# Performance work log

Measured on AMD Instinct MI355X. Metric: run time of the kernel, lower is better.

Reference implementation:

```python
import jax, jax.numpy as jnp
import numpy as np

N, H, G = 8192, 256, 256


def setup_inputs() -> dict:
    key = jax.random.key(0)
    ks = jax.random.split(key, 12)
    s = 1.0 / np.sqrt(H)
    inp = {
        "x": jax.random.normal(ks[0], (N, H), dtype=jnp.float32),
        "batch": jnp.sort(jax.random.randint(ks[1], (N,), 0, G)),
        "num_graphs": G,
        "aw": jax.random.uniform(ks[2], (H, H), jnp.float32, -s, s),
        "ab": jax.random.uniform(ks[3], (H,), jnp.float32, -s, s),
        "p1w": jax.random.uniform(ks[4], (H, H), jnp.float32, -s, s),
        "p1b": jax.random.uniform(ks[5], (H,), jnp.float32, -s, s),
        "p2w": jax.random.uniform(ks[6], (H, H), jnp.float32, -s, s),
        "p2b": jax.random.uniform(ks[7], (H,), jnp.float32, -s, s),
        "r1w": jax.random.uniform(ks[8], (H, H), jnp.float32, -s, s),
        "r1b": jax.random.uniform(ks[9], (H,), jnp.float32, -s, s),
        "r2w": jax.random.uniform(ks[10], (H, H), jnp.float32, -s, s),
        "r2b": jax.random.uniform(ks[11], (H,), jnp.float32, -s, s),
    }
    return inp


def reference(x, batch, num_graphs, aw, ab, p1w, p1b, p2w, p2b, r1w, r1b, r2w, r2b):
    # phi: two Linear+ReLU layers
    h = jax.nn.relu(jax.nn.relu(x @ p1w + p1b) @ p2w + p2b)          # [N, H]
    s = h @ aw + ab                                                  # attention scores [N, H]
    dot = s @ s.T                                                    # [N, N]
    mask = (batch[:, None] == batch[None, :]).astype(dot.dtype)      # block-diagonal [N, N]
    # hand-rolled masked softmax exactly as in the torch module
    max_vals = jnp.max(dot * mask, axis=1, keepdims=True)            # [N, 1]
    masked_dot = (dot - max_vals) * mask
    e = jnp.exp(masked_dot)
    attn = e / jnp.sum(e * mask, axis=1, keepdims=True) * mask       # [N, N]
    x_weighted = attn @ h                                            # [N, H]
    x_agg = jax.ops.segment_sum(x_weighted, batch, num_segments=num_graphs)  # [G, H]
    # rho: two Linear+ReLU layers
    out = jax.nn.relu(jax.nn.relu(x_agg @ r1w + r1b) @ r2w + r2b)    # [G, H]
    return out
```

## Files before the change

kernel.cpp:

```cpp
#include <hip/hip_runtime.h>
#include <hip/hip_bf16.h>
#include <stdint.h>

#define NN 8192
#define HH 256
#define GG 256

typedef __bf16 bf16x8 __attribute__((ext_vector_type(8)));
typedef float f32x4 __attribute__((ext_vector_type(4)));
typedef unsigned short u16v8 __attribute__((ext_vector_type(8)));

__device__ __forceinline__ ushort f2bf(float f) {
  union { float f; uint32_t u; } v; v.f = f;
  uint32_t u = v.u;
  u += 0x7fffu + ((u >> 16) & 1u);
  return (ushort)(u >> 16);
}
__device__ __forceinline__ float bf2f(ushort h) {
  union { uint32_t u; float f; } v; v.u = ((uint32_t)h) << 16;
  return v.f;
}

__global__ __launch_bounds__(512) void k_prep(const float* __restrict__ p1w,
                                              const float* __restrict__ p2w,
                                              const float* __restrict__ aw,
                                              const float* __restrict__ r1w,
                                              const float* __restrict__ r2w,
                                              ushort* __restrict__ wT1,
                                              ushort* __restrict__ wT2,
                                              ushort* __restrict__ wTa,
                                              ushort* __restrict__ rK1,
                                              ushort* __restrict__ rK2) {
  int b = blockIdx.x, t = threadIdx.x;
  if (b < 48) {
    int mat = b >> 4, tile = b & 15;
    int tr = (tile >> 2) * 64, tc = (tile & 3) * 64;
    const float* w = mat == 0 ? p1w : mat == 1 ? p2w : aw;
    ushort* o = mat == 0 ? wT1 : mat == 1 ? wT2 : wTa;
    __shared__ float tileb[64][65];
    int rr = t >> 3, cg = (t & 7) * 8;
    const float* src = w + (size_t)(tr + rr) * HH + tc + cg;
    float4 v0 = *(const float4*)src;
    float4 v1 = *(const float4*)(src + 4);
    float* drow = &tileb[rr][cg];
    drow[0] = v0.x; drow[1] = v0.y; drow[2] = v0.z; drow[3] = v0.w;
    drow[4] = v1.x; drow[5] = v1.y; drow[6] = v1.z; drow[7] = v1.w;
    __syncthreads();
    int rn = t >> 3, kg = (t & 7) * 8;
    u16v8 a;
#pragma unroll
    for (int j = 0; j < 8; ++j) a[j] = f2bf(tileb[kg + j][rn]);
    *(u16v8*)(o + (size_t)(tc + rn) * HH + tr + kg) = a;
  } else {
    int eb = b - 48;
    const float* src = (eb < 8) ? r1w : r2w;
    ushort* dst = (eb < 8) ? rK1 : rK2;
    int sub = eb & 7;
#pragma unroll
    for (int it = 0; it < 2; ++it) {
      int base = sub * 8192 + it * 4096 + t * 8;
      float4 v0 = *(const float4*)(src + base);
      float4 v1 = *(const float4*)(src + base + 4);
      u16v8 o;
      o[0] = f2bf(v0.x); o[1] = f2bf(v0.y); o[2] = f2bf(v0.z); o[3] = f2bf(v0.w);
      o[4] = f2bf(v1.x); o[5] = f2bf(v1.y); o[6] = f2bf(v1.z); o[7] = f2bf(v1.w);
      *(u16v8*)(dst + base) = o;
    }
  }
}

#define LOADQ(SRC, DST)                                                        \
  {                                                                            \
    _Pragma("unroll")                                                          \
    for (int it_ = 0; it_ < 2; ++it_) {                                        \
      int ch_ = it_ * 1024 + tid;                                              \
      int rw_ = ch_ >> 5, c_ = ch_ & 31;                                       \
      int sc_ = (ch_ & ~31) | (c_ ^ (rw_ & 7));                                \
      __builtin_amdgcn_global_load_lds(                                        \
          (const __attribute__((address_space(1))) uint32_t*)((SRC) + sc_ * 8),\
          (__attribute__((address_space(3))) uint32_t*)((DST) + ch_ * 8),      \
          16, 0, 0);                                                           \
    }                                                                          \
  }

__global__ __launch_bounds__(1024) void k_main(
    const float* __restrict__ x, const int* __restrict__ batch,
    const float* __restrict__ ab,
    const float* __restrict__ p1b, const float* __restrict__ p2b,
    const float* __restrict__ r1b, const float* __restrict__ r2b,
    const ushort* __restrict__ wT1, const ushort* __restrict__ wT2,
    const ushort* __restrict__ wTa,
    const ushort* __restrict__ rK1, const ushort* __restrict__ rK2,
    float* __restrict__ out) {
  __shared__ char smem[139808];
  ushort* wq0  = (ushort*)smem;
  ushort* wq1  = (ushort*)(smem + 32768);
  ushort* actA = (ushort*)(smem + 65536);
  ushort* actB = (ushort*)(smem + 98304);
  int*    bb   = (int*)(smem + 131072);
  int*    mm   = (int*)(smem + 132096);
  float*  colw = (float*)(smem + 132128);
  float*  xa   = (float*)(smem + 133152);
  float*  parts= (float*)(smem + 134176);
  float*  pmax = (float*)(smem + 138272);
  float*  psum = (float*)(smem + 138784);
  float*  fct  = (float*)(smem + 139296);

  const int g = blockIdx.x, tid = threadIdx.x;
  const int lane = tid & 63, wid = tid >> 6;
  const int l15 = lane & 15, q = lane >> 4, x7 = l15 & 7;

  if (tid < 256) bb[tid] = batch[tid * 32];
  if (tid == 0) { mm[0] = 256; mm[1] = 256; }
  __syncthreads();
  if (tid < 256) {
    int v = bb[tid];
    int pv = (tid == 0) ? -1 : bb[tid - 1];
    if (v >= g && pv < g) mm[0] = tid;
    if (v >= g + 1 && pv < g + 1) mm[1] = tid;
  }
  __syncthreads();
  {
    int which = -1, v = 0;
    if (tid < 32) { which = 2; v = g; }
    else if (tid >= 64 && tid < 96) { which = 3; v = g + 1; }
    if (which >= 0) {
      int B = mm[which - 2];
      int u = tid & 31;
      if (B == 0) { if (u == 0) mm[which] = 0; }
      else {
        int i = (B - 1) * 32 + 1 + u;
        if (i <= 8191 && batch[i] >= v && batch[i - 1] < v) mm[which] = i;
        if (B == 256 && u == 0 && batch[8191] < v) mm[which] = 8192;
      }
    }
  }
  __syncthreads();
  const int r0 = mm[2];
  int n = mm[3] - r0;
  if (n > 64) n = 64;
  const int nrt = (n + 15) >> 4;
  const int R = nrt * 16;

  LOADQ(wT1, wq0);
  LOADQ(wT1 + 16384, wq1);

  for (int ch = tid; ch < R * 32; ch += 1024) {
    int row = ch >> 5, c = ch & 31;
    int srow = r0 + row; if (srow > 8191) srow = 8191;
    const float* xp = x + (size_t)srow * HH + c * 8;
    float4 v0 = *(const float4*)xp;
    float4 v1 = *(const float4*)(xp + 4);
    u16v8 o;
    o[0] = f2bf(v0.x); o[1] = f2bf(v0.y); o[2] = f2bf(v0.z); o[3] = f2bf(v0.w);
    o[4] = f2bf(v1.x); o[5] = f2bf(v1.y); o[6] = f2bf(v1.z); o[7] = f2bf(v1.w);
    int dst = (ch & ~31) | (c ^ (row & 7));
    *(u16v8*)(actA + dst * 8) = o;
  }
  __syncthreads();

  for (int s = 0; s < 12; ++s) {
    const int L = s >> 2, qd = s & 3;
    const ushort* cur = (s & 1) ? wq1 : wq0;
    if (s >= 1 && s < 11) {
      int sn = s + 1;
      int Ln = sn >> 2, qn = sn & 3;
      const ushort* wtn = (Ln == 0) ? wT1 : (Ln == 1) ? wT2 : wTa;
      ushort* dstb = (sn & 1) ? wq1 : wq0;
      LOADQ(wtn + qn * 16384, dstb);
    }
    const ushort* aIn = (L & 1) ? actB : actA;
    ushort* aOut = (L & 1) ? actA : actB;
    const float* bias = (L == 0) ? p1b : (L == 1) ? p2b : ab;
    const int dorelu = (L < 2);
    if (wid < nrt * 4) {
      int rt = wid >> 2, ct = wid & 3;
      f32x4 acc = {0.f, 0.f, 0.f, 0.f};
#pragma unroll
      for (int kk = 0; kk < 8; ++kk) {
        int kc = (kk * 4 + q) ^ x7;
        bf16x8 a  = *(const bf16x8*)(aIn + ((rt * 16 + l15) * 32 + kc) * 8);
        bf16x8 bf = *(const bf16x8*)(cur + ((ct * 16 + l15) * 32 + kc) * 8);
        acc = __builtin_amdgcn_mfma_f32_16x16x32_bf16(a, bf, acc, 0, 0, 0);
      }
      int col = qd * 64 + ct * 16 + l15;
      float bv = bias[col];
#pragma unroll
      for (int i = 0; i < 4; ++i) {
        float vv = acc[i] + bv;
        if (dorelu) vv = fmaxf(vv, 0.f);
        int r = rt * 16 + q * 4 + i;
        int cc = (col >> 3) ^ (r & 7);
        aOut[(r * 32 + cc) * 8 + (col & 7)] = f2bf(vv);
      }
    }
    __syncthreads();
  }

  if (tid < 256) colw[tid] = 0.f;
  __syncthreads();
  const int rt = wid & 3, h2 = wid >> 2;
  const bool liveW = (wid < 8) && (rt * 16 < n);
  float e0[4], e1[4];
  int cb0 = 0, cb1 = 0;
  if (liveW) {
    const char* stc = (const char*)actB;
    cb0 = (h2 * 2 + 0) * 16; cb1 = (h2 * 2 + 1) * 16;
    f32x4 acc0 = {0.f, 0.f, 0.f, 0.f}, acc1 = acc0;
    const int arow = rt * 16 + l15;
    if (cb0 < n) {
#pragma unroll
      for (int kk = 0; kk < 8; kk++) {
        int kc = ((kk * 4 + q) ^ x7) << 4;
        bf16x8 a  = *(const bf16x8*)(stc + arow * 512 + kc);
        bf16x8 b0 = *(const bf16x8*)(stc + (cb0 + l15) * 512 + kc);
        acc0 = __builtin_amdgcn_mfma_f32_16x16x32_bf16(a, b0, acc0, 0, 0, 0);
        if (cb1 < n) {
          bf16x8 b1 = *(const bf16x8*)(stc + (cb1 + l15) * 512 + kc);
          acc1 = __builtin_amdgcn_mfma_f32_16x16x32_bf16(a, b1, acc1, 0, 0, 0);
        }
      }
    }
    float pm[4], ps[4];
#pragma unroll
    for (int i = 0; i < 4; i++) {
      float mmx = (cb0 + l15 < n) ? acc0[i] : -1e30f;
      if (cb1 + l15 < n) mmx = fmaxf(mmx, acc1[i]);
      pm[i] = mmx;
    }
#pragma unroll
    for (int off = 1; off < 16; off <<= 1)
#pragma unroll
      for (int i = 0; i < 4; i++) pm[i] = fmaxf(pm[i], __shfl_xor(pm[i], off));
#pragma unroll
    for (int i = 0; i < 4; i++) {
      e0[i] = (cb0 + l15 < n) ? __expf(acc0[i] - pm[i]) : 0.f;
      e1[i] = (cb1 + l15 < n) ? __expf(acc1[i] - pm[i]) : 0.f;
      ps[i] = e0[i] + e1[i];
    }
#pragma unroll
    for (int off = 1; off < 16; off <<= 1)
#pragma unroll
      for (int i = 0; i < 4; i++) ps[i] += __shfl_xor(ps[i], off);
    if (l15 == 0) {
#pragma unroll
      for (int i = 0; i < 4; i++) {
        int row = rt * 16 + q * 4 + i;
        pmax[h2 * 64 + row] = pm[i];
        psum[h2 * 64 + row] = ps[i];
      }
    }
  }
  __syncthreads();
  if (tid < 128) {
    int h = tid >> 6, row = tid & 63;
    float m0 = pmax[row], m1 = pmax[64 + row];
    float m = fmaxf(m0, m1);
    float S = psum[row] * __expf(m0 - m) + psum[64 + row] * __expf(m1 - m);
    fct[h * 64 + row] = (S > 0.f) ? __expf(pmax[h * 64 + row] - m) / S : 0.f;
  }
  __syncthreads();
  if (liveW) {
    float cs0 = 0.f, cs1 = 0.f;
#pragma unroll
    for (int i = 0; i < 4; i++) {
      int row = rt * 16 + q * 4 + i;
      if (row < n) {
        float f = fct[h2 * 64 + row];
        cs0 += e0[i] * f;
        cs1 += e1[i] * f;
      }
    }
    cs0 += __shfl_xor(cs0, 16); cs0 += __shfl_xor(cs0, 32);
    cs1 += __shfl_xor(cs1, 16); cs1 += __shfl_xor(cs1, 32);
    if (lane < 16) {
      if (cb0 < n) atomicAdd(&colw[cb0 + l15], cs0);
      if (cb1 < n) atomicAdd(&colw[cb1 + l15], cs1);
    }
  }
  __syncthreads();

  {
    int c = tid & 255, qr = tid >> 8;
    float agg = 0.f;
    for (int jj = qr; jj < n; jj += 4) {
      int cc = (c >> 3) ^ (jj & 7);
      agg = fmaf(colw[jj], bf2f(actA[(jj * 32 + cc) * 8 + (c & 7)]), agg);
    }
    parts[qr * 256 + c] = agg;
  }
  __syncthreads();
  if (tid < 256)
    xa[tid] = (parts[tid] + parts[256 + tid]) + (parts[512 + tid] + parts[768 + tid]);
  __syncthreads();

  {
    const int col = tid & 255, kq = tid >> 8;
    const int k0 = kq * 64;
    float a0 = 0.f, a1 = 0.f, a2 = 0.f, a3 = 0.f;
    const ushort* wp = rK1 + (size_t)k0 * HH + col;
#pragma unroll 4
    for (int k = 0; k < 64; k += 4) {
      a0 = fmaf(xa[k0 + k],     bf2f(wp[(size_t)(k)     * HH]), a0);
      a1 = fmaf(xa[k0 + k + 1], bf2f(wp[(size_t)(k + 1) * HH]), a1);
      a2 = fmaf(xa[k0 + k + 2], bf2f(wp[(size_t)(k + 2) * HH]), a2);
      a3 = fmaf(xa[k0 + k + 3], bf2f(wp[(size_t)(k + 3) * HH]), a3);
    }
    parts[kq * 256 + col] = (a0 + a1) + (a2 + a3);
    __syncthreads();
    if (tid < 256)
      colw[tid] = fmaxf(r1b[tid] + (parts[tid] + parts[256 + tid]) +
                        (parts[512 + tid] + parts[768 + tid]), 0.f);
    __syncthreads();
    a0 = a1 = a2 = a3 = 0.f;
    const ushort* wp2 = rK2 + (size_t)k0 * HH + col;
#pragma unroll 4
    for (int k = 0; k < 64; k += 4) {
      a0 = fmaf(colw[k0 + k],     bf2f(wp2[(size_t)(k)     * HH]), a0);
      a1 = fmaf(colw[k0 + k + 1], bf2f(wp2[(size_t)(k + 1) * HH]), a1);
      a2 = fmaf(colw[k0 + k + 2], bf2f(wp2[(size_t)(k + 2) * HH]), a2);
      a3 = fmaf(colw[k0 + k + 3], bf2f(wp2[(size_t)(k + 3) * HH]), a3);
    }
    parts[kq * 256 + col] = (a0 + a1) + (a2 + a3);
    __syncthreads();
    if (tid < 256)
      out[(size_t)g * HH + tid] = fmaxf(r2b[tid] + (parts[tid] + parts[256 + tid]) +
                                        (parts[512 + tid] + parts[768 + tid]), 0.f);
  }
}

extern "C" void kernel_launch(void* const* d_in, const int* in_sizes, int n_in,
                              void* d_out, int out_size, void* d_ws, size_t ws_size,
                              hipStream_t stream) {
  const float* x   = (const float*)d_in[0];
  const int* batch = (const int*)d_in[1];
  const float* aw  = (const float*)d_in[3];
  const float* ab  = (const float*)d_in[4];
  const float* p1w = (const float*)d_in[5];
  const float* p1b = (const float*)d_in[6];
  const float* p2w = (const float*)d_in[7];
  const float* p2b = (const float*)d_in[8];
  const float* r1w = (const float*)d_in[9];
  const float* r1b = (const float*)d_in[10];
  const float* r2w = (const float*)d_in[11];
  const float* r2b = (const float*)d_in[12];
  float* out = (float*)d_out;

  char* ws = (char*)d_ws;
  ushort* wT1 = (ushort*)(ws);
  ushort* wT2 = wT1 + 65536;
  ushort* wTa = wT2 + 65536;
  ushort* rK1 = wTa + 65536;
  ushort* rK2 = rK1 + 65536;

  k_prep<<<dim3(64), dim3(512), 0, stream>>>(p1w, p2w, aw, r1w, r2w,
                                             wT1, wT2, wTa, rK1, rK2);
  k_main<<<dim3(256), dim3(1024), 0, stream>>>(x, batch, ab, p1b, p2b, r1b, r2b,
                                               wT1, wT2, wTa, rK1, rK2, out);
}
```

Baseline: 33.26 us.

## Move rho MLP into separate batched MFMA kernel over graph rows

The per-graph rho MLP, done as scalar FMA GEMV at the end of each k_main block, is moved into a new k_rho2 kernel. It processes 32 graphs per block with bf16 MFMA, keeping the weights in LDS. The prep kernel now transposes all five weights and pre-swizzles their layout, so the LOADQ address swizzle is removed. This targets the redundant per-block reads of the rho weights and the serial GEMV tail, at the cost of an extra launch, an xagg round trip through global memory, and only 8 blocks in the rho stage.

```diff
diff --git a/kernel.cpp b/kernel.cpp
--- a/kernel.cpp
+++ b/kernel.cpp
@@ -5,6 +5,7 @@
 #define NN 8192
 #define HH 256
 #define GG 256
+#define PR 32
 
 typedef __bf16 bf16x8 __attribute__((ext_vector_type(8)));
 typedef float f32x4 __attribute__((ext_vector_type(4)));
@@ -29,44 +30,29 @@
                                               ushort* __restrict__ wT1,
                                               ushort* __restrict__ wT2,
                                               ushort* __restrict__ wTa,
-                                              ushort* __restrict__ rK1,
-                                              ushort* __restrict__ rK2) {
+                                              ushort* __restrict__ rT1,
+                                              ushort* __restrict__ rT2) {
   int b = blockIdx.x, t = threadIdx.x;
-  if (b < 48) {
-    int mat = b >> 4, tile = b & 15;
-    int tr = (tile >> 2) * 64, tc = (tile & 3) * 64;
-    const float* w = mat == 0 ? p1w : mat == 1 ? p2w : aw;
-    ushort* o = mat == 0 ? wT1 : mat == 1 ? wT2 : wTa;
-    __shared__ float tileb[64][65];
-    int rr = t >> 3, cg = (t & 7) * 8;
-    const float* src = w + (size_t)(tr + rr) * HH + tc + cg;
-    float4 v0 = *(const float4*)src;
-    float4 v1 = *(const float4*)(src + 4);
-    float* drow = &tileb[rr][cg];
-    drow[0] = v0.x; drow[1] = v0.y; drow[2] = v0.z; drow[3] = v0.w;
-    drow[4] = v1.x; drow[5] = v1.y; drow[6] = v1.z; drow[7] = v1.w;
-    __syncthreads();
-    int rn = t >> 3, kg = (t & 7) * 8;
-    u16v8 a;
-#pragma unroll
-    for (int j = 0; j < 8; ++j) a[j] = f2bf(tileb[kg + j][rn]);
-    *(u16v8*)(o + (size_t)(tc + rn) * HH + tr + kg) = a;
-  } else {
-    int eb = b - 48;
-    const float* src = (eb < 8) ? r1w : r2w;
-    ushort* dst = (eb < 8) ? rK1 : rK2;
-    int sub = eb & 7;
-#pragma unroll
-    for (int it = 0; it < 2; ++it) {
-      int base = sub * 8192 + it * 4096 + t * 8;
-      float4 v0 = *(const float4*)(src + base);
-      float4 v1 = *(const float4*)(src + base + 4);
-      u16v8 o;
-      o[0] = f2bf(v0.x); o[1] = f2bf(v0.y); o[2] = f2bf(v0.z); o[3] = f2bf(v0.w);
-      o[4] = f2bf(v1.x); o[5] = f2bf(v1.y); o[6] = f2bf(v1.z); o[7] = f2bf(v1.w);
-      *(u16v8*)(dst + base) = o;
-    }
-  }
+  int mat = b >> 4, tile = b & 15;
+  int tr = (tile >> 2) * 64, tc = (tile & 3) * 64;
+  const float* w = mat == 0 ? p1w : mat == 1 ? p2w : mat == 2 ? aw : mat == 3 ? r1w : r2w;
+  ushort* o = mat == 0 ? wT1 : mat == 1 ? wT2 : mat == 2 ? wTa : mat == 3 ? rT1 : rT2;
+  __shared__ float tileb[64][65];
+  int rr = t >> 3, cg = (t & 7) * 8;
+  const float* src = w + (size_t)(tr + rr) * HH + tc + cg;
+  float4 v0 = *(const float4*)src;
+  float4 v1 = *(const float4*)(src + 4);
+  float* drow = &tileb[rr][cg];
+  drow[0] = v0.x; drow[1] = v0.y; drow[2] = v0.z; drow[3] = v0.w;
+  drow[4] = v1.x; drow[5] = v1.y; drow[6] = v1.z; drow[7] = v1.w;
+  __syncthreads();
+  int rn = t >> 3, kg = (t & 7) * 8;
+  u16v8 a;
+#pragma unroll
+  for (int j = 0; j < 8; ++j) a[j] = f2bf(tileb[kg + j][rn]);
+  int row = tc + rn;
+  int c0 = ((tr + kg) >> 3) ^ (row & 7);
+  *(u16v8*)(o + (size_t)row * HH + c0 * 8) = a;
 }
 
 #define LOADQ(SRC, DST)                                                        \
@@ -74,10 +60,8 @@
     _Pragma("unroll")                                                          \
     for (int it_ = 0; it_ < 2; ++it_) {                                        \
       int ch_ = it_ * 1024 + tid;                                              \
-      int rw_ = ch_ >> 5, c_ = ch_ & 31;                                       \
-      int sc_ = (ch_ & ~31) | (c_ ^ (rw_ & 7));                                \
       __builtin_amdgcn_global_load_lds(                                        \
-          (const __attribute__((address_space(1))) uint32_t*)((SRC) + sc_ * 8),\
+          (const __attribute__((address_space(1))) uint32_t*)((SRC) + ch_ * 8),\
           (__attribute__((address_space(3))) uint32_t*)((DST) + ch_ * 8),      \
           16, 0, 0);                                                           \
     }                                                                          \
@@ -87,11 +71,9 @@
     const float* __restrict__ x, const int* __restrict__ batch,
     const float* __restrict__ ab,
     const float* __restrict__ p1b, const float* __restrict__ p2b,
-    const float* __restrict__ r1b, const float* __restrict__ r2b,
     const ushort* __restrict__ wT1, const ushort* __restrict__ wT2,
     const ushort* __restrict__ wTa,
-    const ushort* __restrict__ rK1, const ushort* __restrict__ rK2,
-    float* __restrict__ out) {
+    float* __restrict__ xagg) {
   __shared__ char smem[139808];
   ushort* wq0  = (ushort*)smem;
   ushort* wq1  = (ushort*)(smem + 32768);
@@ -100,7 +82,6 @@
   int*    bb   = (int*)(smem + 131072);
   int*    mm   = (int*)(smem + 132096);
   float*  colw = (float*)(smem + 132128);
-  float*  xa   = (float*)(smem + 133152);
   float*  parts= (float*)(smem + 134176);
   float*  pmax = (float*)(smem + 138272);
   float*  psum = (float*)(smem + 138784);
@@ -291,41 +272,95 @@
   }
   __syncthreads();
   if (tid < 256)
-    xa[tid] = (parts[tid] + parts[256 + tid]) + (parts[512 + tid] + parts[768 + tid]);
-  __syncthreads();
-
-  {
-    const int col = tid & 255, kq = tid >> 8;
-    const int k0 = kq * 64;
-    float a0 = 0.f, a1 = 0.f, a2 = 0.f, a3 = 0.f;
-    const ushort* wp = rK1 + (size_t)k0 * HH + col;
-#pragma unroll 4
-    for (int k = 0; k < 64; k += 4) {
-      a0 = fmaf(xa[k0 + k],     bf2f(wp[(size_t)(k)     * HH]), a0);
-      a1 = fmaf(xa[k0 + k + 1], bf2f(wp[(size_t)(k + 1) * HH]), a1);
-      a2 = fmaf(xa[k0 + k + 2], bf2f(wp[(size_t)(k + 2) * HH]), a2);
-      a3 = fmaf(xa[k0 + k + 3], bf2f(wp[(size_t)(k + 3) * HH]), a3);
-    }
-    parts[kq * 256 + col] = (a0 + a1) + (a2 + a3);
-    __syncthreads();
-    if (tid < 256)
-      colw[tid] = fmaxf(r1b[tid] + (parts[tid] + parts[256 + tid]) +
-                        (parts[512 + tid] + parts[768 + tid]), 0.f);
-    __syncthreads();
-    a0 = a1 = a2 = a3 = 0.f;
-    const ushort* wp2 = rK2 + (size_t)k0 * HH + col;
-#pragma unroll 4
-    for (int k = 0; k < 64; k += 4) {
-      a0 = fmaf(colw[k0 + k],     bf2f(wp2[(size_t)(k)     * HH]), a0);
-      a1 = fmaf(colw[k0 + k + 1], bf2f(wp2[(size_t)(k + 1) * HH]), a1);
-      a2 = fmaf(colw[k0 + k + 2], bf2f(wp2[(size_t)(k + 2) * HH]), a2);
-      a3 = fmaf(colw[k0 + k + 3], bf2f(wp2[(size_t)(k + 3) * HH]), a3);
-    }
-    parts[kq * 256 + col] = (a0 + a1) + (a2 + a3);
-    __syncthreads();
-    if (tid < 256)
-      out[(size_t)g * HH + tid] = fmaxf(r2b[tid] + (parts[tid] + parts[256 + tid]) +
-                                        (parts[512 + tid] + parts[768 + tid]), 0.f);
+    xagg[(size_t)g * HH + tid] = (parts[tid] + parts[256 + tid]) +
+                                 (parts[512 + tid] + parts[768 + tid]);
+}
+
+__device__ __forceinline__ void load_w_lin(const ushort* __restrict__ wt,
+                                           ushort* wl, int tid) {
+#pragma unroll
+  for (int it = 0; it < 16; ++it) {
+    int chunk = it * 512 + tid;
+    __builtin_amdgcn_global_load_lds(
+        (const __attribute__((address_space(1))) uint32_t*)(wt + chunk * 8),
+        (__attribute__((address_space(3))) uint32_t*)(wl + chunk * 8),
+        16, 0, 0);
+  }
+}
+
+#define PHI_MFMA(ACC)                                                          \
+  {                                                                            \
+    _Pragma("unroll")                                                          \
+    for (int kk = 0; kk < 8; ++kk) {                                           \
+      int kc = (kk * 4 + q) ^ x7;                                              \
+      bf16x8 a = *(const bf16x8*)(act + ((wr + l15) * 32 + kc) * 8);           \
+      _Pragma("unroll")                                                        \
+      for (int nt = 0; nt < 4; ++nt) {                                         \
+        bf16x8 bfr = *(const bf16x8*)(wl + ((wc + nt * 16 + l15) * 32 + kc) * 8);\
+        ACC[nt] = __builtin_amdgcn_mfma_f32_16x16x32_bf16(a, bfr, ACC[nt], 0, 0, 0); \
+      }                                                                        \
+    }                                                                          \
+  }
+
+__global__ __launch_bounds__(512, 1) void k_rho2(const float* __restrict__ xagg,
+    const ushort* __restrict__ rt1, const float* __restrict__ b1,
+    const ushort* __restrict__ rt2, const float* __restrict__ b2,
+    float* __restrict__ out) {
+  __shared__ ushort wl[HH * HH];
+  __shared__ ushort act[PR * HH];
+  const int tid = threadIdx.x;
+  const int rowbase = blockIdx.x * PR;
+
+  load_w_lin(rt1, wl, tid);
+
+#pragma unroll
+  for (int it = 0; it < 2; ++it) {
+    int chunk = it * 512 + tid;
+    int row = chunk >> 5, c = chunk & 31;
+    const float* xp = xagg + (size_t)(rowbase + row) * HH + c * 8;
+    float4 v0 = *(const float4*)xp;
+    float4 v1 = *(const float4*)(xp + 4);
+    u16v8 o;
+    o[0] = f2bf(v0.x); o[1] = f2bf(v0.y); o[2] = f2bf(v0.z); o[3] = f2bf(v0.w);
+    o[4] = f2bf(v1.x); o[5] = f2bf(v1.y); o[6] = f2bf(v1.z); o[7] = f2bf(v1.w);
+    int dst = (chunk & ~31) | (c ^ (row & 7));
+    *(u16v8*)(act + dst * 8) = o;
+  }
+  __syncthreads();
+
+  const int lane = tid & 63, wid = tid >> 6;
+  const int l15 = lane & 15, q = lane >> 4, x7 = l15 & 7;
+  const int wr = (wid & 1) * 16;
+  const int wc = (wid >> 1) * 64;
+  const int ro = wr + q * 4;
+
+  f32x4 acc[4] = {{0.f,0.f,0.f,0.f},{0.f,0.f,0.f,0.f},{0.f,0.f,0.f,0.f},{0.f,0.f,0.f,0.f}};
+  PHI_MFMA(acc);
+  __syncthreads();
+  load_w_lin(rt2, wl, tid);
+#pragma unroll
+  for (int nt = 0; nt < 4; ++nt) {
+    int col = wc + nt * 16 + l15;
+    float bv = b1[col];
+#pragma unroll
+    for (int i = 0; i < 4; ++i) {
+      float v = fmaxf(acc[nt][i] + bv, 0.f);
+      int r = ro + i;
+      int cc = (col >> 3) ^ (r & 7);
+      act[(r * 32 + cc) * 8 + (col & 7)] = f2bf(v);
+    }
+  }
+  __syncthreads();
+
+  f32x4 acc2[4] = {{0.f,0.f,0.f,0.f},{0.f,0.f,0.f,0.f},{0.f,0.f,0.f,0.f},{0.f,0.f,0.f,0.f}};
+  PHI_MFMA(acc2);
+#pragma unroll
+  for (int nt = 0; nt < 4; ++nt) {
+    int col = wc + nt * 16 + l15;
+    float bv = b2[col];
+#pragma unroll
+    for (int i = 0; i < 4; ++i)
+      out[(size_t)(rowbase + ro + i) * HH + col] = fmaxf(acc2[nt][i] + bv, 0.f);
   }
 }
 
@@ -350,11 +385,13 @@
   ushort* wT1 = (ushort*)(ws);
   ushort* wT2 = wT1 + 65536;
   ushort* wTa = wT2 + 65536;
-  ushort* rK1 = wTa + 65536;
-  ushort* rK2 = rK1 + 65536;
-
-  k_prep<<<dim3(64), dim3(512), 0, stream>>>(p1w, p2w, aw, r1w, r2w,
-                                             wT1, wT2, wTa, rK1, rK2);
-  k_main<<<dim3(256), dim3(1024), 0, stream>>>(x, batch, ab, p1b, p2b, r1b, r2b,
-                                               wT1, wT2, wTa, rK1, rK2, out);
-}
+  ushort* rT1 = wTa + 65536;
+  ushort* rT2 = rT1 + 65536;
+  float*  xagg = (float*)(ws + (size_t)5 * 131072);
+
+  k_prep<<<dim3(80), dim3(512), 0, stream>>>(p1w, p2w, aw, r1w, r2w,
+                                             wT1, wT2, wTa, rT1, rT2);
+  k_main<<<dim3(256), dim3(1024), 0, stream>>>(x, batch, ab, p1b, p2b,
+                                               wT1, wT2, wTa, xagg);
+  k_rho2<<<dim3(8), dim3(512), 0, stream>>>(xagg, rT1, r1b, rT2, r2b, out);
+}
```

Result: slower. 36.59 us (+10.0%).

## Hold MLP weights in registers per wave instead of staging quarters through LDS

Applied to the files above, without the earlier changes.

The three per-graph 256x256 layers (phi1, phi2, attention projection) no longer stream weight quarters into double-buffered LDS over twelve synchronised steps. Each of the 16 waves now owns a 16-column slice, loads its weight fragments straight from global memory into registers (prefetching the next layer's weights early), and loops over up to four row tiles. This drops 64 KB of LDS and cuts the barriers from twelve to three. In exchange it raises VGPR pressure (two sets of 8 bf16x8 fragments per lane) and issues uncoalesced-ish per-lane global weight loads that every block repeats.

```diff
diff --git a/kernel.cpp b/kernel.cpp
--- a/kernel.cpp
+++ b/kernel.cpp
@@ -69,20 +69,6 @@
   }
 }
 
-#define LOADQ(SRC, DST)                                                        \
-  {                                                                            \
-    _Pragma("unroll")                                                          \
-    for (int it_ = 0; it_ < 2; ++it_) {                                        \
-      int ch_ = it_ * 1024 + tid;                                              \
-      int rw_ = ch_ >> 5, c_ = ch_ & 31;                                       \
-      int sc_ = (ch_ & ~31) | (c_ ^ (rw_ & 7));                                \
-      __builtin_amdgcn_global_load_lds(                                        \
-          (const __attribute__((address_space(1))) uint32_t*)((SRC) + sc_ * 8),\
-          (__attribute__((address_space(3))) uint32_t*)((DST) + ch_ * 8),      \
-          16, 0, 0);                                                           \
-    }                                                                          \
-  }
-
 __global__ __launch_bounds__(1024) void k_main(
     const float* __restrict__ x, const int* __restrict__ batch,
     const float* __restrict__ ab,
@@ -92,19 +78,16 @@
     const ushort* __restrict__ wTa,
     const ushort* __restrict__ rK1, const ushort* __restrict__ rK2,
     float* __restrict__ out) {
-  __shared__ char smem[139808];
-  ushort* wq0  = (ushort*)smem;
-  ushort* wq1  = (ushort*)(smem + 32768);
-  ushort* actA = (ushort*)(smem + 65536);
-  ushort* actB = (ushort*)(smem + 98304);
-  int*    bb   = (int*)(smem + 131072);
-  int*    mm   = (int*)(smem + 132096);
-  float*  colw = (float*)(smem + 132128);
-  float*  xa   = (float*)(smem + 133152);
-  float*  parts= (float*)(smem + 134176);
-  float*  pmax = (float*)(smem + 138272);
-  float*  psum = (float*)(smem + 138784);
-  float*  fct  = (float*)(smem + 139296);
+  __shared__ ushort actA[16384];
+  __shared__ ushort actB[16384];
+  __shared__ int bb[256];
+  __shared__ int mm[4];
+  __shared__ float colw[256];
+  __shared__ float xa[256];
+  __shared__ float parts[1024];
+  __shared__ float pmax[128];
+  __shared__ float psum[128];
+  __shared__ float fct[128];
 
   const int g = blockIdx.x, tid = threadIdx.x;
   const int lane = tid & 63, wid = tid >> 6;
@@ -139,11 +122,7 @@
   const int r0 = mm[2];
   int n = mm[3] - r0;
   if (n > 64) n = 64;
-  const int nrt = (n + 15) >> 4;
-  const int R = nrt * 16;
-
-  LOADQ(wT1, wq0);
-  LOADQ(wT1 + 16384, wq1);
+  const int R = ((n + 15) >> 4) * 16;
 
   for (int ch = tid; ch < R * 32; ch += 1024) {
     int row = ch >> 5, c = ch & 31;
@@ -159,43 +138,89 @@
   }
   __syncthreads();
 
-  for (int s = 0; s < 12; ++s) {
-    const int L = s >> 2, qd = s & 3;
-    const ushort* cur = (s & 1) ? wq1 : wq0;
-    if (s >= 1 && s < 11) {
-      int sn = s + 1;
-      int Ln = sn >> 2, qn = sn & 3;
-      const ushort* wtn = (Ln == 0) ? wT1 : (Ln == 1) ? wT2 : wTa;
-      ushort* dstb = (sn & 1) ? wq1 : wq0;
-      LOADQ(wtn + qn * 16384, dstb);
-    }
-    const ushort* aIn = (L & 1) ? actB : actA;
-    ushort* aOut = (L & 1) ? actA : actB;
-    const float* bias = (L == 0) ? p1b : (L == 1) ? p2b : ab;
-    const int dorelu = (L < 2);
-    if (wid < nrt * 4) {
-      int rt = wid >> 2, ct = wid & 3;
-      f32x4 acc = {0.f, 0.f, 0.f, 0.f};
-#pragma unroll
-      for (int kk = 0; kk < 8; ++kk) {
-        int kc = (kk * 4 + q) ^ x7;
-        bf16x8 a  = *(const bf16x8*)(aIn + ((rt * 16 + l15) * 32 + kc) * 8);
-        bf16x8 bf = *(const bf16x8*)(cur + ((ct * 16 + l15) * 32 + kc) * 8);
-        acc = __builtin_amdgcn_mfma_f32_16x16x32_bf16(a, bf, acc, 0, 0, 0);
-      }
-      int col = qd * 64 + ct * 16 + l15;
-      float bv = bias[col];
-#pragma unroll
-      for (int i = 0; i < 4; ++i) {
-        float vv = acc[i] + bv;
-        if (dorelu) vv = fmaxf(vv, 0.f);
-        int r = rt * 16 + q * 4 + i;
-        int cc = (col >> 3) ^ (r & 7);
-        aOut[(r * 32 + cc) * 8 + (col & 7)] = f2bf(vv);
-      }
-    }
-    __syncthreads();
-  }
+  const int mycol = wid * 16 + l15;
+  const ushort* wrow1 = wT1 + (size_t)mycol * HH + q * 8;
+  const ushort* wrow2 = wT2 + (size_t)mycol * HH + q * 8;
+  const ushort* wrowa = wTa + (size_t)mycol * HH + q * 8;
+  bf16x8 wA[8], wB[8];
+#pragma unroll
+  for (int kk = 0; kk < 8; ++kk) wA[kk] = *(const bf16x8*)(wrow1 + kk * 32);
+#pragma unroll
+  for (int kk = 0; kk < 8; ++kk) wB[kk] = *(const bf16x8*)(wrow2 + kk * 32);
+
+  {
+    float bv = p1b[mycol];
+#pragma unroll
+    for (int rt4 = 0; rt4 < 4; ++rt4) {
+      if (rt4 * 16 < n) {
+        f32x4 acc = {0.f, 0.f, 0.f, 0.f};
+#pragma unroll
+        for (int kk = 0; kk < 8; ++kk) {
+          int ca = (kk * 4 + q) ^ x7;
+          bf16x8 a = *(const bf16x8*)(actA + ((rt4 * 16 + l15) * 32 + ca) * 8);
+          acc = __builtin_amdgcn_mfma_f32_16x16x32_bf16(a, wA[kk], acc, 0, 0, 0);
+        }
+#pragma unroll
+        for (int i = 0; i < 4; ++i) {
+          float vv = fmaxf(acc[i] + bv, 0.f);
+          int r = rt4 * 16 + q * 4 + i;
+          int cc = (mycol >> 3) ^ (r & 7);
+          actB[(r * 32 + cc) * 8 + (mycol & 7)] = f2bf(vv);
+        }
+      }
+    }
+  }
+  __syncthreads();
+#pragma unroll
+  for (int kk = 0; kk < 8; ++kk) wA[kk] = *(const bf16x8*)(wrowa + kk * 32);
+
+  {
+    float bv = p2b[mycol];
+#pragma unroll
+    for (int rt4 = 0; rt4 < 4; ++rt4) {
+      if (rt4 * 16 < n) {
+        f32x4 acc = {0.f, 0.f, 0.f, 0.f};
+#pragma unroll
+        for (int kk = 0; kk < 8; ++kk) {
+          int ca = (kk * 4 + q) ^ x7;
+          bf16x8 a = *(const bf16x8*)(actB + ((rt4 * 16 + l15) * 32 + ca) * 8);
+          acc = __builtin_amdgcn_mfma_f32_16x16x32_bf16(a, wB[kk], acc, 0, 0, 0);
+        }
+#pragma unroll
+        for (int i = 0; i < 4; ++i) {
+          float vv = fmaxf(acc[i] + bv, 0.f);
+          int r = rt4 * 16 + q * 4 + i;
+          int cc = (mycol >> 3) ^ (r & 7);
+          actA[(r * 32 + cc) * 8 + (mycol & 7)] = f2bf(vv);
+        }
+      }
+    }
+  }
+  __syncthreads();
+
+  {
+    float bv = ab[mycol];
+#pragma unroll
+    for (int rt4 = 0; rt4 < 4; ++rt4) {
+      if (rt4 * 16 < n) {
+        f32x4 acc = {0.f, 0.f, 0.f, 0.f};
+#pragma unroll
+        for (int kk = 0; kk < 8; ++kk) {
+          int ca = (kk * 4 + q) ^ x7;
+          bf16x8 a = *(const bf16x8*)(actA + ((rt4 * 16 + l15) * 32 + ca) * 8);
+          acc = __builtin_amdgcn_mfma_f32_16x16x32_bf16(a, wA[kk], acc, 0, 0, 0);
+        }
+#pragma unroll
+        for (int i = 0; i < 4; ++i) {
+          float vv = acc[i] + bv;
+          int r = rt4 * 16 + q * 4 + i;
+          int cc = (mycol >> 3) ^ (r & 7);
+          actB[(r * 32 + cc) * 8 + (mycol & 7)] = f2bf(vv);
+        }
+      }
+    }
+  }
+  __syncthreads();
 
   if (tid < 256) colw[tid] = 0.f;
   __syncthreads();
```

After: 34.01 us. 2.3% more time.
